# Performance work log

Hardware: AMD Instinct MI355X
Metric: run time of the kernel (lower is better)

Reference implementation:

```python
import jax, jax.numpy as jnp
import numpy as np

N = 100000       # nodes
E = 1600000      # edges (before self loops)
F_IN = 128       # num_node_features
D = 64           # conv_dim == label_dimension
G = 64           # global_dim
NG = 64          # num_graphs in batch


def _lin(key, fi, fo):
    kw, kb = jax.random.split(key)
    w = (jax.random.normal(kw, (fi, fo)) / np.float32(np.sqrt(fi))).astype(jnp.float32)
    b = (jax.random.normal(kb, (fo,)) * 0.01).astype(jnp.float32)
    return w, b


def setup_inputs() -> dict:
    key = jax.random.key(0)
    ks = jax.random.split(key, 12)
    x = jax.random.normal(ks[0], (N, F_IN), jnp.float32)
    edge_index = jax.random.randint(ks[1], (2, E), 0, N, dtype=jnp.int32)
    graph_indices = jnp.sort(jax.random.randint(ks[2], (N,), 0, NG, dtype=jnp.int32))
    glob_init = jax.random.normal(ks[3], (1, G), jnp.float32)
    w_nn1, b_nn1 = _lin(ks[4], F_IN, D)
    w_gn1, b_gn1 = _lin(ks[5], G, D)
    w_gg1, b_gg1 = _lin(ks[6], G, G)
    w_ng1, b_ng1 = _lin(ks[7], D, G)
    w_nn2, b_nn2 = _lin(ks[8], D, D)
    w_gn2, b_gn2 = _lin(ks[9], G, D)
    w_gg2, b_gg2 = _lin(ks[10], G, G)
    w_ng2, b_ng2 = _lin(ks[11], D, G)
    return dict(x=x, edge_index=edge_index, graph_indices=graph_indices,
                glob_init=glob_init,
                w_nn1=w_nn1, b_nn1=b_nn1, w_gn1=w_gn1, b_gn1=b_gn1,
                w_gg1=w_gg1, b_gg1=b_gg1, w_ng1=w_ng1, b_ng1=b_ng1,
                w_nn2=w_nn2, b_nn2=b_nn2, w_gn2=w_gn2, b_gn2=b_gn2,
                w_gg2=w_gg2, b_gg2=b_gg2, w_ng2=w_ng2, b_ng2=b_ng2)


def _gcn_glob_layer(xn, glob, row, col, graph_indices, params):
    # GCNConv_glob.forward. row/col already include self loops.
    w_nn, b_nn, w_gn, b_gn, w_gg, b_gg, w_ng, b_ng = params
    h = xn @ w_nn + b_nn                                   # [N, out]
    globs = glob @ w_gn + b_gn                             # [NG, out]
    # binary_matrix @ globs == one-hot gather by graph id
    h = h + globs[graph_indices]
    n = h.shape[0]
    deg = jax.ops.segment_sum(jnp.ones_like(col, dtype=h.dtype), col, num_segments=n)
    dinv = jnp.where(deg > 0, deg, 1.0) ** -0.5
    dinv = jnp.where(deg > 0, dinv, 0.0)
    norm = dinv[row] * dinv[col]                           # [E+N]
    msg = norm[:, None] * h[row]                           # gather + scale
    h = jax.ops.segment_sum(msg, col, num_segments=n)      # scatter-add
    glob2 = glob @ w_gg + b_gg
    parts = jax.ops.segment_max(h, graph_indices, num_segments=NG,
                                indices_are_sorted=True)   # scatter-max readout
    glob2 = glob2 + parts @ w_ng + b_ng
    return h, glob2


def reference(x, edge_index, graph_indices, glob_init,
              w_nn1, b_nn1, w_gn1, b_gn1, w_gg1, b_gg1, w_ng1, b_ng1,
              w_nn2, b_nn2, w_gn2, b_gn2, w_gg2, b_gg2, w_ng2, b_ng2):
    n = x.shape[0]
    loops = jnp.arange(n, dtype=edge_index.dtype)
    row = jnp.concatenate([edge_index[0], loops])          # add_self_loops
    col = jnp.concatenate([edge_index[1], loops])
    glob = jnp.tile(glob_init, (NG, 1))
    h, glob = _gcn_glob_layer(x, glob, row, col, graph_indices,
                              (w_nn1, b_nn1, w_gn1, b_gn1, w_gg1, b_gg1, w_ng1, b_ng1))
    h = jax.nn.relu(h)
    h, glob = _gcn_glob_layer(h, glob, row, col, graph_indices,
                              (w_nn2, b_nn2, w_gn2, b_gn2, w_gg2, b_gg2, w_ng2, b_ng2))
    return jax.nn.sigmoid(h)
```

## Files before the change

kernel.cpp:

```cpp
#include <hip/hip_runtime.h>
#include <math.h>

#define NN 100000
#define EE 1600000
#define FIN 128
#define DD 64
#define NG 64
#define NBINS ((NN + 255) / 256)
#define CH 8192
#define HCH 8192

typedef unsigned int uint;
typedef unsigned short ushort;

__device__ __forceinline__ unsigned f2ord(float f) {
  unsigned u = __float_as_uint(f);
  return (u & 0x80000000u) ? ~u : (u | 0x80000000u);
}
__device__ __forceinline__ float ord2f(unsigned m) {
  unsigned u = (m & 0x80000000u) ? (m & 0x7FFFFFFFu) : ~m;
  return __uint_as_float(u);
}
__device__ __forceinline__ float bflo(uint v) { return __uint_as_float(v << 16); }
__device__ __forceinline__ float bfhi(uint v) { return __uint_as_float(v & 0xffff0000u); }
__device__ __forceinline__ uint bfr(float x) {
  uint u = __float_as_uint(x);
  return (u + 0x7fffu + ((u >> 16) & 1u)) >> 16;
}
__device__ __forceinline__ uint packbf(float lo, float hi) { return bfr(lo) | (bfr(hi) << 16); }

__global__ __launch_bounds__(256) void bin_hist(const int* __restrict__ col,
                                                int* __restrict__ bin_cnt, int e) {
  __shared__ int hist[NBINS];
  int tid = threadIdx.x;
  for (int i = tid; i < NBINS; i += 256) hist[i] = 0;
  __syncthreads();
  int s = blockIdx.x * HCH;
  int eend = s + HCH < e ? s + HCH : e;
  for (int i = s + tid; i < eend; i += 256) {
    int c = __builtin_nontemporal_load(&col[i]);
    atomicAdd(&hist[c >> 8], 1);
  }
  __syncthreads();
  for (int i = tid; i < NBINS; i += 256)
    if (hist[i]) atomicAdd(&bin_cnt[i], hist[i]);
}

__global__ __launch_bounds__(512) void bin_scan(const int* __restrict__ bin_cnt,
    int* __restrict__ bstart, int* __restrict__ bcur) {
  __shared__ int s[512];
  int tid = threadIdx.x;
  int v = (tid < NBINS) ? bin_cnt[tid] : 0;
  s[tid] = v;
  __syncthreads();
  for (int off = 1; off < 512; off <<= 1) {
    int t = (tid >= off) ? s[tid - off] : 0;
    __syncthreads();
    s[tid] += t;
    __syncthreads();
  }
  if (tid < NBINS) {
    int st = s[tid] - v;
    bstart[tid] = st;
    bcur[tid] = st;
  }
  if (tid == NBINS - 1) bstart[NBINS] = s[tid];
}

__global__ __launch_bounds__(256) void pass1_bin(const int* __restrict__ row,
    const int* __restrict__ col, int* __restrict__ bin_cursor,
    uint* __restrict__ temp, int e) {
  __shared__ int hist[NBINS];
  __shared__ int base[NBINS];
  int tid = threadIdx.x;
  int s = blockIdx.x * CH;
  int colr[32];
  #pragma unroll
  for (int it = 0; it < 32; ++it) {
    int i = s + tid + it * 256;
    colr[it] = (i < e) ? __builtin_nontemporal_load(&col[i]) : -1;
  }
  for (int i = tid; i < NBINS; i += 256) hist[i] = 0;
  __syncthreads();
  #pragma unroll
  for (int it = 0; it < 32; ++it)
    if (colr[it] >= 0) atomicAdd(&hist[colr[it] >> 8], 1);
  __syncthreads();
  for (int i = tid; i < NBINS; i += 256) {
    int cnt = hist[i];
    base[i] = cnt ? atomicAdd(&bin_cursor[i], cnt) : 0;
    hist[i] = 0;
  }
  __syncthreads();
  #pragma unroll
  for (int it = 0; it < 32; ++it) {
    int c = colr[it];
    if (c >= 0) {
      int i = s + tid + it * 256;
      int r = __builtin_nontemporal_load(&row[i]);
      int b = c >> 8;
      int pos = base[b] + atomicAdd(&hist[b], 1);
      temp[pos] = ((uint)r << 8) | (uint)(c & 255);
    }
  }
}

__global__ __launch_bounds__(256) void pass2_scatter(const uint* __restrict__ temp,
    const int* __restrict__ bstart, int* __restrict__ cursor0,
    int* __restrict__ deg, float* __restrict__ dinv,
    int* __restrict__ csr, int n) {
  __shared__ int hist[256];
  __shared__ int sc[256];
  __shared__ int cur[256];
  int b = blockIdx.x;
  int tid = threadIdx.x;
  int s = bstart[b], eend = bstart[b + 1];
  hist[tid] = 0;
  __syncthreads();
  for (int i = s + tid; i < eend; i += 256)
    atomicAdd(&hist[temp[i] & 255u], 1);
  __syncthreads();
  int v = hist[tid];
  sc[tid] = v;
  __syncthreads();
  for (int off = 1; off < 256; off <<= 1) {
    int t = (tid >= off) ? sc[tid - off] : 0;
    __syncthreads();
    sc[tid] += t;
    __syncthreads();
  }
  int st = s + sc[tid] - v;
  cur[tid] = st;
  int node = b * 256 + tid;
  if (node < n) {
    cursor0[node] = st;
    deg[node] = v;
    dinv[node] = rsqrtf((float)v + 1.0f);
  }
  __syncthreads();
  for (int i = s + tid; i < eend; i += 256) {
    uint rec = temp[i];
    int pos = atomicAdd(&cur[rec & 255u], 1);
    csr[pos] = (int)(rec >> 8);
  }
}

__global__ void glob1_kernel(const float* __restrict__ gi, const float* __restrict__ w,
                             const float* __restrict__ b, float* __restrict__ out) {
  int j = threadIdx.x;
  float acc = b[j];
  for (int k = 0; k < 64; ++k) acc += gi[k] * w[k * 64 + j];
  out[j] = acc;
}

__global__ __launch_bounds__(256) void gemm1(const float* __restrict__ x,
    const float* __restrict__ w, const float* __restrict__ b,
    const float* __restrict__ g1, const float* __restrict__ dinv,
    uint* __restrict__ hbf, int n) {
  __shared__ float XsT[FIN][64];
  __shared__ float Ws[FIN][DD];
  int base = blockIdx.x * 64;
  if (blockIdx.x == 0 && threadIdx.x < 32) hbf[(size_t)n * 32 + threadIdx.x] = 0u;
  const float4* w4 = (const float4*)w;
  float4* ws4 = (float4*)Ws;
  for (int idx = threadIdx.x; idx < FIN * DD / 4; idx += 256) ws4[idx] = w4[idx];
  const float4* x4 = (const float4*)x;
  for (int idx = threadIdx.x; idx < 64 * FIN / 4; idx += 256) {
    int kq = idx & 31, r = idx >> 5;
    int gr = base + r;
    float4 v = make_float4(0.f, 0.f, 0.f, 0.f);
    if (gr < n) v = x4[gr * 32 + kq];
    int k0 = kq * 4, s = k0 & 60;
    XsT[k0 + 0][r ^ s] = v.x;
    XsT[k0 + 1][r ^ s] = v.y;
    XsT[k0 + 2][r ^ s] = v.z;
    XsT[k0 + 3][r ^ s] = v.w;
  }
  __syncthreads();
  int tx = threadIdx.x & 15, ty = threadIdx.x >> 4;
  float acc[4][4] = {};
  #pragma unroll 4
  for (int k = 0; k < FIN; ++k) {
    float4 av = *(const float4*)&XsT[k][(4 * ty) ^ (k & 60)];
    float4 bv = *(const float4*)&Ws[k][4 * tx];
    float ax[4] = {av.x, av.y, av.z, av.w};
    float bx[4] = {bv.x, bv.y, bv.z, bv.w};
    #pragma unroll
    for (int i = 0; i < 4; ++i)
      #pragma unroll
      for (int j = 0; j < 4; ++j)
        acc[i][j] += ax[i] * bx[j];
  }
  float bias[4];
  #pragma unroll
  for (int j = 0; j < 4; ++j) bias[j] = b[4 * tx + j] + g1[4 * tx + j];
  #pragma unroll
  for (int i = 0; i < 4; ++i) {
    int row = base + 4 * ty + i;
    if (row < n) {
      float dv = dinv[row];
      hbf[row * 32 + 2 * tx]     = packbf(dv * (acc[i][0] + bias[0]), dv * (acc[i][1] + bias[1]));
      hbf[row * 32 + 2 * tx + 1] = packbf(dv * (acc[i][2] + bias[2]), dv * (acc[i][3] + bias[3]));
    }
  }
}

__global__ __launch_bounds__(256) void gemm2(const uint* __restrict__ hbf,
    const float* __restrict__ w, const float* __restrict__ bb,
    const float* __restrict__ globs2, const int* __restrict__ gidx,
    const float* __restrict__ dinv, uint* __restrict__ obf, int n) {
  __shared__ float XsT[DD][64];
  __shared__ float Ws[DD][DD];
  int base = blockIdx.x * 64;
  const float4* w4 = (const float4*)w;
  float4* ws4 = (float4*)Ws;
  for (int idx = threadIdx.x; idx < DD * DD / 4; idx += 256) ws4[idx] = w4[idx];
  const uint2* h2 = (const uint2*)hbf;
  for (int idx = threadIdx.x; idx < 64 * DD / 4; idx += 256) {
    int kq = idx & 15, r = idx >> 4;
    int gr = base + r;
    uint2 v = make_uint2(0u, 0u);
    if (gr < n) v = h2[gr * 16 + kq];
    int k0 = kq * 4, s = k0 & 60;
    XsT[k0 + 0][r ^ s] = fmaxf(bflo(v.x), 0.f);
    XsT[k0 + 1][r ^ s] = fmaxf(bfhi(v.x), 0.f);
    XsT[k0 + 2][r ^ s] = fmaxf(bflo(v.y), 0.f);
    XsT[k0 + 3][r ^ s] = fmaxf(bfhi(v.y), 0.f);
  }
  __syncthreads();
  int tx = threadIdx.x & 15, ty = threadIdx.x >> 4;
  float acc[4][4] = {};
  #pragma unroll 4
  for (int k = 0; k < DD; ++k) {
    float4 av = *(const float4*)&XsT[k][(4 * ty) ^ (k & 60)];
    float4 bv = *(const float4*)&Ws[k][4 * tx];
    float ax[4] = {av.x, av.y, av.z, av.w};
    float bx[4] = {bv.x, bv.y, bv.z, bv.w};
    #pragma unroll
    for (int i = 0; i < 4; ++i)
      #pragma unroll
      for (int j = 0; j < 4; ++j)
        acc[i][j] += ax[i] * bx[j];
  }
  #pragma unroll
  for (int i = 0; i < 4; ++i) {
    int row = base + 4 * ty + i;
    if (row < n) {
      const float* gl = globs2 + gidx[row] * 64 + 4 * tx;
      float dv = dinv[row];
      float c0 = acc[i][0] + bb[4 * tx + 0] + gl[0];
      float c1 = acc[i][1] + bb[4 * tx + 1] + gl[1];
      float c2 = acc[i][2] + bb[4 * tx + 2] + gl[2];
      float c3 = acc[i][3] + bb[4 * tx + 3] + gl[3];
      obf[row * 32 + 2 * tx]     = packbf(dv * c0, dv * c1);
      obf[row * 32 + 2 * tx + 1] = packbf(dv * c2, dv * c3);
    }
  }
}

template <int SIG>
__global__ __launch_bounds__(256) void gather_agg(const int* __restrict__ csr,
    const int* __restrict__ cursor0, const int* __restrict__ deg,
    const float* __restrict__ dinv, const uint* __restrict__ h,
    void* __restrict__ outv, int n) {
  int node = blockIdx.x * 4 + (threadIdx.x >> 6);
  if (node >= n) return;
  int lane = threadIdx.x & 63;
  int q = lane >> 4;
  int fq = lane & 15;
  int start = cursor0[node];
  int end = start + deg[node];
  int last = end - 1;
  const uint2* h2 = (const uint2*)h;
  float a0 = 0.f, a1 = 0.f, a2 = 0.f, a3 = 0.f;
  for (int e = start + q; e < end; e += 16) {
    #pragma unroll
    for (int j = 0; j < 4; ++j) {
      int i = e + 4 * j;
      int ic = i < last ? i : last;
      int r = __builtin_nontemporal_load(&csr[ic]);
      r = (i < end) ? r : n;
      uint2 v = h2[r * 16 + fq];
      a0 += bflo(v.x); a1 += bfhi(v.x);
      a2 += bflo(v.y); a3 += bfhi(v.y);
    }
  }
  if (q == 0) {
    uint2 v = h2[node * 16 + fq];
    a0 += bflo(v.x); a1 += bfhi(v.x);
    a2 += bflo(v.y); a3 += bfhi(v.y);
  }
  a0 += __shfl_xor(a0, 16); a0 += __shfl_xor(a0, 32);
  a1 += __shfl_xor(a1, 16); a1 += __shfl_xor(a1, 32);
  a2 += __shfl_xor(a2, 16); a2 += __shfl_xor(a2, 32);
  a3 += __shfl_xor(a3, 16); a3 += __shfl_xor(a3, 32);
  if (q == 0) {
    float di = dinv[node];
    a0 *= di; a1 *= di; a2 *= di; a3 *= di;
    if (SIG) {
      float4 o;
      o.x = 1.f / (1.f + __expf(-a0));
      o.y = 1.f / (1.f + __expf(-a1));
      o.z = 1.f / (1.f + __expf(-a2));
      o.w = 1.f / (1.f + __expf(-a3));
      ((float4*)outv)[node * 16 + fq] = o;
    } else {
      uint2 o;
      o.x = packbf(a0, a1);
      o.y = packbf(a2, a3);
      ((uint2*)outv)[node * 16 + fq] = o;
    }
  }
}

__global__ void seg_max(const ushort* __restrict__ B, const int* __restrict__ gidx,
                        unsigned* __restrict__ parts_ord, int n, int chunk) {
  int f = threadIdx.x;
  int start = blockIdx.x * chunk;
  int end = start + chunk; if (end > n) end = n;
  if (start >= end) return;
  int curg = gidx[start];
  float m = -INFINITY;
  for (int i = start; i < end; ++i) {
    int g = gidx[i];
    if (g != curg) {
      atomicMax(&parts_ord[curg * 64 + f], f2ord(m));
      curg = g; m = -INFINITY;
    }
    m = fmaxf(m, __uint_as_float(((uint)B[i * 64 + f]) << 16));
  }
  atomicMax(&parts_ord[curg * 64 + f], f2ord(m));
}

__global__ void glob2_kernel(const float* __restrict__ gi, const unsigned* __restrict__ parts_ord,
    const float* __restrict__ w_gg1, const float* __restrict__ b_gg1,
    const float* __restrict__ w_ng1, const float* __restrict__ b_ng1,
    const float* __restrict__ w_gn2, const float* __restrict__ b_gn2,
    float* __restrict__ globs2) {
  __shared__ float t[64];
  int g = blockIdx.x, j = threadIdx.x;
  float acc = b_gg1[j] + b_ng1[j];
  for (int k = 0; k < 64; ++k) acc += gi[k] * w_gg1[k * 64 + j];
  for (int k = 0; k < 64; ++k) acc += ord2f(parts_ord[g * 64 + k]) * w_ng1[k * 64 + j];
  t[j] = acc;
  __syncthreads();
  float acc2 = b_gn2[j];
  for (int k = 0; k < 64; ++k) acc2 += t[k] * w_gn2[k * 64 + j];
  globs2[g * 64 + j] = acc2;
}

extern "C" void kernel_launch(void* const* d_in, const int* in_sizes, int n_in,
                              void* d_out, int out_size, void* d_ws, size_t ws_size,
                              hipStream_t stream) {
  const float* x         = (const float*)d_in[0];
  const int*   ei        = (const int*)d_in[1];
  const int*   gidx      = (const int*)d_in[2];
  const float* glob_init = (const float*)d_in[3];
  const float* w_nn1 = (const float*)d_in[4];  const float* b_nn1 = (const float*)d_in[5];
  const float* w_gn1 = (const float*)d_in[6];  const float* b_gn1 = (const float*)d_in[7];
  const float* w_gg1 = (const float*)d_in[8];  const float* b_gg1 = (const float*)d_in[9];
  const float* w_ng1 = (const float*)d_in[10]; const float* b_ng1 = (const float*)d_in[11];
  const float* w_nn2 = (const float*)d_in[12]; const float* b_nn2 = (const float*)d_in[13];
  const float* w_gn2 = (const float*)d_in[14]; const float* b_gn2 = (const float*)d_in[15];

  const int* row = ei;
  const int* col = ei + EE;

  char* p = (char*)d_ws;
  int*      deg    = (int*)p;       p += ((NN * 4 + 255) & ~255);
  float*    dinv   = (float*)p;     p += ((NN * 4 + 255) & ~255);
  int*      cursor = (int*)p;       p += ((NN * 4 + 255) & ~255);
  int*      bcnt   = (int*)p;       p += ((NBINS * 4 + 255) & ~255);
  int*      bstart = (int*)p;       p += (((NBINS + 1) * 4 + 255) & ~255);
  int*      bcur   = (int*)p;       p += ((NBINS * 4 + 255) & ~255);
  uint*     temp   = (uint*)p;      p += (size_t)EE * 4;
  int*      csr    = (int*)p;       p += (size_t)EE * 4;
  uint*     A      = (uint*)p;      p += (size_t)(NN + 1) * 32 * 4;
  unsigned* parts  = (unsigned*)p;  p += NG * 64 * 4;
  float*    g1     = (float*)p;     p += 256;
  float*    globs2 = (float*)p;
  uint*     B      = (uint*)d_out;
  float*    out    = (float*)d_out;

  hipMemsetAsync(bcnt, 0, NBINS * 4, stream);
  bin_hist<<<(EE + HCH - 1) / HCH, 256, 0, stream>>>(col, bcnt, EE);
  bin_scan<<<1, 512, 0, stream>>>(bcnt, bstart, bcur);
  pass1_bin<<<(EE + CH - 1) / CH, 256, 0, stream>>>(row, col, bcur, temp, EE);
  pass2_scatter<<<NBINS, 256, 0, stream>>>(temp, bstart, cursor, deg, dinv, csr, NN);

  glob1_kernel<<<1, 64, 0, stream>>>(glob_init, w_gn1, b_gn1, g1);
  gemm1<<<(NN + 63) / 64, 256, 0, stream>>>(x, w_nn1, b_nn1, g1, dinv, A, NN);
  gather_agg<0><<<(NN + 3) / 4, 256, 0, stream>>>(csr, cursor, deg, dinv, A, (void*)B, NN);

  hipMemsetAsync(parts, 0, NG * 64 * 4, stream);
  seg_max<<<(NN + 63) / 64, 64, 0, stream>>>((const ushort*)B, gidx, parts, NN, 64);
  glob2_kernel<<<NG, 64, 0, stream>>>(glob_init, parts, w_gg1, b_gg1, w_ng1, b_ng1,
                                      w_gn2, b_gn2, globs2);

  gemm2<<<(NN + 63) / 64, 256, 0, stream>>>(B, w_nn2, b_nn2, globs2, gidx, dinv, A, NN);
  gather_agg<1><<<(NN + 3) / 4, 256, 0, stream>>>(csr, cursor, deg, dinv, A, (void*)out, NN);
}
```

Baseline: 274.2 us.

## Split node features into two planes and pad CSR rows for branchless gather

```diff
diff --git a/kernel.cpp b/kernel.cpp
--- a/kernel.cpp
+++ b/kernel.cpp
@@ -9,6 +9,7 @@
 #define NBINS ((NN + 255) / 256)
 #define CH 8192
 #define HCH 8192
+#define PADSLACK 768
 
 typedef unsigned int uint;
 typedef unsigned short ushort;
@@ -115,13 +116,15 @@
   int b = blockIdx.x;
   int tid = threadIdx.x;
   int s = bstart[b], eend = bstart[b + 1];
+  int csr_base = s + PADSLACK * b;
   hist[tid] = 0;
   __syncthreads();
   for (int i = s + tid; i < eend; i += 256)
     atomicAdd(&hist[temp[i] & 255u], 1);
   __syncthreads();
   int v = hist[tid];
-  sc[tid] = v;
+  int vp = (v + 3) & ~3;
+  sc[tid] = vp;
   __syncthreads();
   for (int off = 1; off < 256; off <<= 1) {
     int t = (tid >= off) ? sc[tid - off] : 0;
@@ -129,7 +132,7 @@
     sc[tid] += t;
     __syncthreads();
   }
-  int st = s + sc[tid] - v;
+  int st = csr_base + sc[tid] - vp;
   cur[tid] = st;
   int node = b * 256 + tid;
   if (node < n) {
@@ -137,6 +140,7 @@
     deg[node] = v;
     dinv[node] = rsqrtf((float)v + 1.0f);
   }
+  for (int i = st + v; i < st + vp; ++i) csr[i] = n;
   __syncthreads();
   for (int i = s + tid; i < eend; i += 256) {
     uint rec = temp[i];
@@ -159,8 +163,10 @@
     uint* __restrict__ hbf, int n) {
   __shared__ float XsT[FIN][64];
   __shared__ float Ws[FIN][DD];
+  const size_t PL = (size_t)(NN + 1) * 16;
   int base = blockIdx.x * 64;
-  if (blockIdx.x == 0 && threadIdx.x < 32) hbf[(size_t)n * 32 + threadIdx.x] = 0u;
+  if (blockIdx.x == 0 && threadIdx.x < 32)
+    hbf[(size_t)(threadIdx.x >> 4) * PL + (size_t)n * 16 + (threadIdx.x & 15)] = 0u;
   const float4* w4 = (const float4*)w;
   float4* ws4 = (float4*)Ws;
   for (int idx = threadIdx.x; idx < FIN * DD / 4; idx += 256) ws4[idx] = w4[idx];
@@ -194,13 +200,16 @@
   float bias[4];
   #pragma unroll
   for (int j = 0; j < 4; ++j) bias[j] = b[4 * tx + j] + g1[4 * tx + j];
+  size_t pbase = (tx >= 8) ? PL : 0;
+  int within = (2 * tx) & 15;
   #pragma unroll
   for (int i = 0; i < 4; ++i) {
     int row = base + 4 * ty + i;
     if (row < n) {
       float dv = dinv[row];
-      hbf[row * 32 + 2 * tx]     = packbf(dv * (acc[i][0] + bias[0]), dv * (acc[i][1] + bias[1]));
-      hbf[row * 32 + 2 * tx + 1] = packbf(dv * (acc[i][2] + bias[2]), dv * (acc[i][3] + bias[3]));
+      uint* dst = hbf + pbase + (size_t)row * 16 + within;
+      dst[0] = packbf(dv * (acc[i][0] + bias[0]), dv * (acc[i][1] + bias[1]));
+      dst[1] = packbf(dv * (acc[i][2] + bias[2]), dv * (acc[i][3] + bias[3]));
     }
   }
 }
@@ -211,16 +220,20 @@
     const float* __restrict__ dinv, uint* __restrict__ obf, int n) {
   __shared__ float XsT[DD][64];
   __shared__ float Ws[DD][DD];
+  const size_t BS = (size_t)NN * 16;
+  const size_t PL = (size_t)(NN + 1) * 16;
   int base = blockIdx.x * 64;
   const float4* w4 = (const float4*)w;
   float4* ws4 = (float4*)Ws;
   for (int idx = threadIdx.x; idx < DD * DD / 4; idx += 256) ws4[idx] = w4[idx];
-  const uint2* h2 = (const uint2*)hbf;
   for (int idx = threadIdx.x; idx < 64 * DD / 4; idx += 256) {
     int kq = idx & 15, r = idx >> 4;
     int gr = base + r;
     uint2 v = make_uint2(0u, 0u);
-    if (gr < n) v = h2[gr * 16 + kq];
+    if (gr < n) {
+      const uint2* src = (const uint2*)(hbf + ((kq >= 8) ? BS : 0));
+      v = src[(size_t)gr * 8 + (kq & 7)];
+    }
     int k0 = kq * 4, s = k0 & 60;
     XsT[k0 + 0][r ^ s] = fmaxf(bflo(v.x), 0.f);
     XsT[k0 + 1][r ^ s] = fmaxf(bfhi(v.x), 0.f);
@@ -242,6 +255,8 @@
       for (int j = 0; j < 4; ++j)
         acc[i][j] += ax[i] * bx[j];
   }
+  size_t pbase = (tx >= 8) ? PL : 0;
+  int within = (2 * tx) & 15;
   #pragma unroll
   for (int i = 0; i < 4; ++i) {
     int row = base + 4 * ty + i;
@@ -252,8 +267,9 @@
       float c1 = acc[i][1] + bb[4 * tx + 1] + gl[1];
       float c2 = acc[i][2] + bb[4 * tx + 2] + gl[2];
       float c3 = acc[i][3] + bb[4 * tx + 3] + gl[3];
-      obf[row * 32 + 2 * tx]     = packbf(dv * c0, dv * c1);
-      obf[row * 32 + 2 * tx + 1] = packbf(dv * c2, dv * c3);
+      uint* dst = obf + pbase + (size_t)row * 16 + within;
+      dst[0] = packbf(dv * c0, dv * c1);
+      dst[1] = packbf(dv * c2, dv * c3);
     }
   }
 }
@@ -263,52 +279,45 @@
     const int* __restrict__ cursor0, const int* __restrict__ deg,
     const float* __restrict__ dinv, const uint* __restrict__ h,
     void* __restrict__ outv, int n) {
-  int node = blockIdx.x * 4 + (threadIdx.x >> 6);
+  int plane = blockIdx.x & 1;
+  int chunk = blockIdx.x >> 1;
+  int node = chunk * 4 + (threadIdx.x >> 6);
   if (node >= n) return;
   int lane = threadIdx.x & 63;
   int q = lane >> 4;
   int fq = lane & 15;
   int start = cursor0[node];
-  int end = start + deg[node];
-  int last = end - 1;
-  const uint2* h2 = (const uint2*)h;
-  float a0 = 0.f, a1 = 0.f, a2 = 0.f, a3 = 0.f;
-  for (int e = start + q; e < end; e += 16) {
+  int dp = (deg[node] + 3) & ~3;
+  const uint* hp = h + (size_t)plane * ((size_t)(NN + 1) * 16);
+  float a0 = 0.f, a1 = 0.f;
+  for (int g = q * 4; g < dp; g += 16) {
+    const int* cp = csr + start + g;
     #pragma unroll
     for (int j = 0; j < 4; ++j) {
-      int i = e + 4 * j;
-      int ic = i < last ? i : last;
-      int r = __builtin_nontemporal_load(&csr[ic]);
-      r = (i < end) ? r : n;
-      uint2 v = h2[r * 16 + fq];
-      a0 += bflo(v.x); a1 += bfhi(v.x);
-      a2 += bflo(v.y); a3 += bfhi(v.y);
+      int r = __builtin_nontemporal_load(&cp[j]);
+      uint v = hp[(size_t)r * 16 + fq];
+      a0 += bflo(v);
+      a1 += bfhi(v);
     }
   }
   if (q == 0) {
-    uint2 v = h2[node * 16 + fq];
-    a0 += bflo(v.x); a1 += bfhi(v.x);
-    a2 += bflo(v.y); a3 += bfhi(v.y);
+    uint v = hp[(size_t)node * 16 + fq];
+    a0 += bflo(v);
+    a1 += bfhi(v);
   }
   a0 += __shfl_xor(a0, 16); a0 += __shfl_xor(a0, 32);
   a1 += __shfl_xor(a1, 16); a1 += __shfl_xor(a1, 32);
-  a2 += __shfl_xor(a2, 16); a2 += __shfl_xor(a2, 32);
-  a3 += __shfl_xor(a3, 16); a3 += __shfl_xor(a3, 32);
   if (q == 0) {
     float di = dinv[node];
-    a0 *= di; a1 *= di; a2 *= di; a3 *= di;
+    a0 *= di; a1 *= di;
     if (SIG) {
-      float4 o;
+      float2 o;
       o.x = 1.f / (1.f + __expf(-a0));
       o.y = 1.f / (1.f + __expf(-a1));
-      o.z = 1.f / (1.f + __expf(-a2));
-      o.w = 1.f / (1.f + __expf(-a3));
-      ((float4*)outv)[node * 16 + fq] = o;
+      ((float2*)((float*)outv + (size_t)node * 64 + plane * 32))[fq] = o;
     } else {
-      uint2 o;
-      o.x = packbf(a0, a1);
-      o.y = packbf(a2, a3);
-      ((uint2*)outv)[node * 16 + fq] = o;
+      ((uint*)outv)[(size_t)plane * ((size_t)NN * 16) + (size_t)node * 16 + fq] =
+          packbf(a0, a1);
     }
   }
 }
@@ -316,6 +325,7 @@
 __global__ void seg_max(const ushort* __restrict__ B, const int* __restrict__ gidx,
                         unsigned* __restrict__ parts_ord, int n, int chunk) {
   int f = threadIdx.x;
+  const ushort* Bp = B + (size_t)(f >> 5) * ((size_t)NN * 32) + (f & 31);
   int start = blockIdx.x * chunk;
   int end = start + chunk; if (end > n) end = n;
   if (start >= end) return;
@@ -327,7 +337,7 @@
       atomicMax(&parts_ord[curg * 64 + f], f2ord(m));
       curg = g; m = -INFINITY;
     }
-    m = fmaxf(m, __uint_as_float(((uint)B[i * 64 + f]) << 16));
+    m = fmaxf(m, __uint_as_float(((uint)Bp[(size_t)i * 32]) << 16));
   }
   atomicMax(&parts_ord[curg * 64 + f], f2ord(m));
 }
@@ -374,8 +384,8 @@
   int*      bstart = (int*)p;       p += (((NBINS + 1) * 4 + 255) & ~255);
   int*      bcur   = (int*)p;       p += ((NBINS * 4 + 255) & ~255);
   uint*     temp   = (uint*)p;      p += (size_t)EE * 4;
-  int*      csr    = (int*)p;       p += (size_t)EE * 4;
-  uint*     A      = (uint*)p;      p += (size_t)(NN + 1) * 32 * 4;
+  int*      csr    = (int*)p;       p += (size_t)(EE + PADSLACK * NBINS) * 4;
+  uint*     A      = (uint*)p;      p += (size_t)2 * (NN + 1) * 16 * 4;
   unsigned* parts  = (unsigned*)p;  p += NG * 64 * 4;
   float*    g1     = (float*)p;     p += 256;
   float*    globs2 = (float*)p;
@@ -390,7 +400,7 @@
 
   glob1_kernel<<<1, 64, 0, stream>>>(glob_init, w_gn1, b_gn1, g1);
   gemm1<<<(NN + 63) / 64, 256, 0, stream>>>(x, w_nn1, b_nn1, g1, dinv, A, NN);
-  gather_agg<0><<<(NN + 3) / 4, 256, 0, stream>>>(csr, cursor, deg, dinv, A, (void*)B, NN);
+  gather_agg<0><<<((NN + 3) / 4) * 2, 256, 0, stream>>>(csr, cursor, deg, dinv, A, (void*)B, NN);
 
   hipMemsetAsync(parts, 0, NG * 64 * 4, stream);
   seg_max<<<(NN + 63) / 64, 64, 0, stream>>>((const ushort*)B, gidx, parts, NN, 64);
@@ -398,5 +408,5 @@
                                       w_gn2, b_gn2, globs2);
 
   gemm2<<<(NN + 63) / 64, 256, 0, stream>>>(B, w_nn2, b_nn2, globs2, gidx, dinv, A, NN);
-  gather_agg<1><<<(NN + 3) / 4, 256, 0, stream>>>(csr, cursor, deg, dinv, A, (void*)out, NN);
-}
+  gather_agg<1><<<((NN + 3) / 4) * 2, 256, 0, stream>>>(csr, cursor, deg, dinv, A, (void*)out, NN);
+}
```

Result: slower. 351.9 us (+28.3%).

## Enlarge GEMM row tiles to 128, K-chunk gemm1, fold glob1 into gemm1

Applied to the files above, without the earlier changes.

```diff
diff --git a/kernel.cpp b/kernel.cpp
--- a/kernel.cpp
+++ b/kernel.cpp
@@ -145,62 +145,69 @@
   }
 }
 
-__global__ void glob1_kernel(const float* __restrict__ gi, const float* __restrict__ w,
-                             const float* __restrict__ b, float* __restrict__ out) {
-  int j = threadIdx.x;
-  float acc = b[j];
-  for (int k = 0; k < 64; ++k) acc += gi[k] * w[k * 64 + j];
-  out[j] = acc;
-}
-
 __global__ __launch_bounds__(256) void gemm1(const float* __restrict__ x,
     const float* __restrict__ w, const float* __restrict__ b,
-    const float* __restrict__ g1, const float* __restrict__ dinv,
+    const float* __restrict__ gi, const float* __restrict__ w_gn1,
+    const float* __restrict__ b_gn1, const float* __restrict__ dinv,
     uint* __restrict__ hbf, int n) {
-  __shared__ float XsT[FIN][64];
-  __shared__ float Ws[FIN][DD];
-  int base = blockIdx.x * 64;
-  if (blockIdx.x == 0 && threadIdx.x < 32) hbf[(size_t)n * 32 + threadIdx.x] = 0u;
+  __shared__ float XsT[64][128];
+  __shared__ float Ws[64][DD];
+  __shared__ float g1s[64];
+  int tid = threadIdx.x;
+  int base = blockIdx.x * 128;
+  if (blockIdx.x == 0 && tid >= 64 && tid < 96)
+    hbf[(size_t)n * 32 + (tid - 64)] = 0u;
+  if (tid < 64) {
+    float a = b_gn1[tid];
+    for (int k = 0; k < 64; ++k) a += gi[k] * w_gn1[k * 64 + tid];
+    g1s[tid] = a;
+  }
+  int tx = tid & 15, ty = tid >> 4;
+  float acc[8][4] = {};
+  const float4* x4 = (const float4*)x;
   const float4* w4 = (const float4*)w;
-  float4* ws4 = (float4*)Ws;
-  for (int idx = threadIdx.x; idx < FIN * DD / 4; idx += 256) ws4[idx] = w4[idx];
-  const float4* x4 = (const float4*)x;
-  for (int idx = threadIdx.x; idx < 64 * FIN / 4; idx += 256) {
-    int kq = idx & 31, r = idx >> 5;
-    int gr = base + r;
-    float4 v = make_float4(0.f, 0.f, 0.f, 0.f);
-    if (gr < n) v = x4[gr * 32 + kq];
-    int k0 = kq * 4, s = k0 & 60;
-    XsT[k0 + 0][r ^ s] = v.x;
-    XsT[k0 + 1][r ^ s] = v.y;
-    XsT[k0 + 2][r ^ s] = v.z;
-    XsT[k0 + 3][r ^ s] = v.w;
-  }
-  __syncthreads();
-  int tx = threadIdx.x & 15, ty = threadIdx.x >> 4;
-  float acc[4][4] = {};
-  #pragma unroll 4
-  for (int k = 0; k < FIN; ++k) {
-    float4 av = *(const float4*)&XsT[k][(4 * ty) ^ (k & 60)];
-    float4 bv = *(const float4*)&Ws[k][4 * tx];
-    float ax[4] = {av.x, av.y, av.z, av.w};
-    float bx[4] = {bv.x, bv.y, bv.z, bv.w};
-    #pragma unroll
-    for (int i = 0; i < 4; ++i)
+  #pragma unroll
+  for (int c = 0; c < 2; ++c) {
+    __syncthreads();
+    for (int idx = tid; idx < 1024; idx += 256)
+      ((float4*)Ws)[idx] = w4[c * 1024 + idx];
+    for (int idx = tid; idx < 2048; idx += 256) {
+      int kq = idx & 15, r = idx >> 4;
+      int gr = base + r;
+      float4 v = make_float4(0.f, 0.f, 0.f, 0.f);
+      if (gr < n) v = x4[(size_t)gr * 32 + c * 16 + kq];
+      int k0 = kq * 4, s = k0 & 60;
+      XsT[k0 + 0][r ^ s] = v.x;
+      XsT[k0 + 1][r ^ s] = v.y;
+      XsT[k0 + 2][r ^ s] = v.z;
+      XsT[k0 + 3][r ^ s] = v.w;
+    }
+    __syncthreads();
+    #pragma unroll 4
+    for (int k = 0; k < 64; ++k) {
+      int s = k & 60;
+      float4 alo = *(const float4*)&XsT[k][(8 * ty) ^ s];
+      float4 ahi = *(const float4*)&XsT[k][(8 * ty + 4) ^ s];
+      float4 bv  = *(const float4*)&Ws[k][4 * tx];
+      float ax[8] = {alo.x, alo.y, alo.z, alo.w, ahi.x, ahi.y, ahi.z, ahi.w};
+      float bx[4] = {bv.x, bv.y, bv.z, bv.w};
       #pragma unroll
-      for (int j = 0; j < 4; ++j)
-        acc[i][j] += ax[i] * bx[j];
+      for (int i = 0; i < 8; ++i)
+        #pragma unroll
+        for (int j = 0; j < 4; ++j)
+          acc[i][j] += ax[i] * bx[j];
+    }
   }
   float bias[4];
   #pragma unroll
-  for (int j = 0; j < 4; ++j) bias[j] = b[4 * tx + j] + g1[4 * tx + j];
-  #pragma unroll
-  for (int i = 0; i < 4; ++i) {
-    int row = base + 4 * ty + i;
+  for (int j = 0; j < 4; ++j) bias[j] = b[4 * tx + j] + g1s[4 * tx + j];
+  #pragma unroll
+  for (int i = 0; i < 8; ++i) {
+    int row = base + 8 * ty + i;
     if (row < n) {
       float dv = dinv[row];
-      hbf[row * 32 + 2 * tx]     = packbf(dv * (acc[i][0] + bias[0]), dv * (acc[i][1] + bias[1]));
-      hbf[row * 32 + 2 * tx + 1] = packbf(dv * (acc[i][2] + bias[2]), dv * (acc[i][3] + bias[3]));
+      hbf[(size_t)row * 32 + 2 * tx]     = packbf(dv * (acc[i][0] + bias[0]), dv * (acc[i][1] + bias[1]));
+      hbf[(size_t)row * 32 + 2 * tx + 1] = packbf(dv * (acc[i][2] + bias[2]), dv * (acc[i][3] + bias[3]));
     }
   }
 }
@@ -209,42 +216,45 @@
     const float* __restrict__ w, const float* __restrict__ bb,
     const float* __restrict__ globs2, const int* __restrict__ gidx,
     const float* __restrict__ dinv, uint* __restrict__ obf, int n) {
-  __shared__ float XsT[DD][64];
-  __shared__ float Ws[DD][DD];
-  int base = blockIdx.x * 64;
+  __shared__ float XsT[64][128];
+  __shared__ float Ws[64][DD];
+  int tid = threadIdx.x;
+  int base = blockIdx.x * 128;
   const float4* w4 = (const float4*)w;
-  float4* ws4 = (float4*)Ws;
-  for (int idx = threadIdx.x; idx < DD * DD / 4; idx += 256) ws4[idx] = w4[idx];
+  for (int idx = tid; idx < 1024; idx += 256)
+    ((float4*)Ws)[idx] = w4[idx];
   const uint2* h2 = (const uint2*)hbf;
-  for (int idx = threadIdx.x; idx < 64 * DD / 4; idx += 256) {
+  for (int idx = tid; idx < 2048; idx += 256) {
     int kq = idx & 15, r = idx >> 4;
     int gr = base + r;
     uint2 v = make_uint2(0u, 0u);
-    if (gr < n) v = h2[gr * 16 + kq];
+    if (gr < n) v = h2[(size_t)gr * 16 + kq];
     int k0 = kq * 4, s = k0 & 60;
     XsT[k0 + 0][r ^ s] = fmaxf(bflo(v.x), 0.f);
     XsT[k0 + 1][r ^ s] = fmaxf(bfhi(v.x), 0.f);
     XsT[k0 + 2][r ^ s] = fmaxf(bflo(v.y), 0.f);
     XsT[k0 + 3][r ^ s] = fmaxf(bfhi(v.y), 0.f);
   }
-  __syncthreads();
-  int tx = threadIdx.x & 15, ty = threadIdx.x >> 4;
-  float acc[4][4] = {};
+  int tx = tid & 15, ty = tid >> 4;
+  __syncthreads();
+  float acc[8][4] = {};
   #pragma unroll 4
-  for (int k = 0; k < DD; ++k) {
-    float4 av = *(const float4*)&XsT[k][(4 * ty) ^ (k & 60)];
-    float4 bv = *(const float4*)&Ws[k][4 * tx];
-    float ax[4] = {av.x, av.y, av.z, av.w};
+  for (int k = 0; k < 64; ++k) {
+    int s = k & 60;
+    float4 alo = *(const float4*)&XsT[k][(8 * ty) ^ s];
+    float4 ahi = *(const float4*)&XsT[k][(8 * ty + 4) ^ s];
+    float4 bv  = *(const float4*)&Ws[k][4 * tx];
+    float ax[8] = {alo.x, alo.y, alo.z, alo.w, ahi.x, ahi.y, ahi.z, ahi.w};
     float bx[4] = {bv.x, bv.y, bv.z, bv.w};
     #pragma unroll
-    for (int i = 0; i < 4; ++i)
+    for (int i = 0; i < 8; ++i)
       #pragma unroll
       for (int j = 0; j < 4; ++j)
         acc[i][j] += ax[i] * bx[j];
   }
   #pragma unroll
-  for (int i = 0; i < 4; ++i) {
-    int row = base + 4 * ty + i;
+  for (int i = 0; i < 8; ++i) {
+    int row = base + 8 * ty + i;
     if (row < n) {
       const float* gl = globs2 + gidx[row] * 64 + 4 * tx;
       float dv = dinv[row];
@@ -252,8 +262,8 @@
       float c1 = acc[i][1] + bb[4 * tx + 1] + gl[1];
       float c2 = acc[i][2] + bb[4 * tx + 2] + gl[2];
       float c3 = acc[i][3] + bb[4 * tx + 3] + gl[3];
-      obf[row * 32 + 2 * tx]     = packbf(dv * c0, dv * c1);
-      obf[row * 32 + 2 * tx + 1] = packbf(dv * c2, dv * c3);
+      obf[(size_t)row * 32 + 2 * tx]     = packbf(dv * c0, dv * c1);
+      obf[(size_t)row * 32 + 2 * tx + 1] = packbf(dv * c2, dv * c3);
     }
   }
 }
@@ -280,13 +290,13 @@
       int ic = i < last ? i : last;
       int r = __builtin_nontemporal_load(&csr[ic]);
       r = (i < end) ? r : n;
-      uint2 v = h2[r * 16 + fq];
+      uint2 v = h2[(size_t)r * 16 + fq];
       a0 += bflo(v.x); a1 += bfhi(v.x);
       a2 += bflo(v.y); a3 += bfhi(v.y);
     }
   }
   if (q == 0) {
-    uint2 v = h2[node * 16 + fq];
+    uint2 v = h2[(size_t)node * 16 + fq];
     a0 += bflo(v.x); a1 += bfhi(v.x);
     a2 += bflo(v.y); a3 += bfhi(v.y);
   }
@@ -303,12 +313,12 @@
       o.y = 1.f / (1.f + __expf(-a1));
       o.z = 1.f / (1.f + __expf(-a2));
       o.w = 1.f / (1.f + __expf(-a3));
-      ((float4*)outv)[node * 16 + fq] = o;
+      ((float4*)outv)[(size_t)node * 16 + fq] = o;
     } else {
       uint2 o;
       o.x = packbf(a0, a1);
       o.y = packbf(a2, a3);
-      ((uint2*)outv)[node * 16 + fq] = o;
+      ((uint2*)outv)[(size_t)node * 16 + fq] = o;
     }
   }
 }
@@ -327,7 +337,7 @@
       atomicMax(&parts_ord[curg * 64 + f], f2ord(m));
       curg = g; m = -INFINITY;
     }
-    m = fmaxf(m, __uint_as_float(((uint)B[i * 64 + f]) << 16));
+    m = fmaxf(m, __uint_as_float(((uint)B[(size_t)i * 64 + f]) << 16));
   }
   atomicMax(&parts_ord[curg * 64 + f], f2ord(m));
 }
@@ -377,7 +387,6 @@
   int*      csr    = (int*)p;       p += (size_t)EE * 4;
   uint*     A      = (uint*)p;      p += (size_t)(NN + 1) * 32 * 4;
   unsigned* parts  = (unsigned*)p;  p += NG * 64 * 4;
-  float*    g1     = (float*)p;     p += 256;
   float*    globs2 = (float*)p;
   uint*     B      = (uint*)d_out;
   float*    out    = (float*)d_out;
@@ -388,8 +397,8 @@
   pass1_bin<<<(EE + CH - 1) / CH, 256, 0, stream>>>(row, col, bcur, temp, EE);
   pass2_scatter<<<NBINS, 256, 0, stream>>>(temp, bstart, cursor, deg, dinv, csr, NN);
 
-  glob1_kernel<<<1, 64, 0, stream>>>(glob_init, w_gn1, b_gn1, g1);
-  gemm1<<<(NN + 63) / 64, 256, 0, stream>>>(x, w_nn1, b_nn1, g1, dinv, A, NN);
+  gemm1<<<(NN + 127) / 128, 256, 0, stream>>>(x, w_nn1, b_nn1, glob_init, w_gn1, b_gn1,
+                                              dinv, A, NN);
   gather_agg<0><<<(NN + 3) / 4, 256, 0, stream>>>(csr, cursor, deg, dinv, A, (void*)B, NN);
 
   hipMemsetAsync(parts, 0, NG * 64 * 4, stream);
@@ -397,6 +406,6 @@
   glob2_kernel<<<NG, 64, 0, stream>>>(glob_init, parts, w_gg1, b_gg1, w_ng1, b_ng1,
                                       w_gn2, b_gn2, globs2);
 
-  gemm2<<<(NN + 63) / 64, 256, 0, stream>>>(B, w_nn2, b_nn2, globs2, gidx, dinv, A, NN);
+  gemm2<<<(NN + 127) / 128, 256, 0, stream>>>(B, w_nn2, b_nn2, globs2, gidx, dinv, A, NN);
   gather_agg<1><<<(NN + 3) / 4, 256, 0, stream>>>(csr, cursor, deg, dinv, A, (void*)out, NN);
 }
```

Result: no change. 274.5 us (+0.1%).
